# Optimization experiments

Measured on AMD Instinct MI355X. Metric: run time of the kernel, lower is better.

The kernel has to match this reference:

```python
import jax, jax.numpy as jnp
import numpy as np

B, S, L, H, D, FF, V = 2, 1024, 12, 12, 768, 3072, 50265
DH = D // H
W1 = 256                      # one-sided window (attention_window=512)
MOTIF = (31 + 96 + 80) * 2    # 414
MAXPOS = 4098
EPS = 1e-5
NEG = jnp.float32(-1e9)


def _ln(x, s, b):
    m = jnp.mean(x, -1, keepdims=True)
    v = jnp.mean(jnp.square(x - m), -1, keepdims=True)
    return (x - m) * jax.lax.rsqrt(v + EPS) * s + b


def setup_inputs() -> dict:
    key = jax.random.key(0)
    ks = iter(jax.random.split(key, 48))
    n = lambda *sh: jax.random.normal(next(ks), sh, jnp.float32) * 0.02
    return {
        "input_ids": jax.random.randint(next(ks), (B, S), 0, V),
        "attention_mask": jnp.ones((B, S), jnp.int32),
        "motif_dist": jax.random.uniform(next(ks), (B, MOTIF), dtype=jnp.float32),
        "emb_word": n(V, D), "emb_pos": n(MAXPOS, D), "emb_type": n(1, D),
        "emb_ln_s": jnp.ones((D,)), "emb_ln_b": jnp.zeros((D,)),
        "Wq": n(L, D, D), "bq": jnp.zeros((L, D)),
        "Wk": n(L, D, D), "bk": jnp.zeros((L, D)),
        "Wv": n(L, D, D), "bv": jnp.zeros((L, D)),
        "Wqg": n(L, D, D), "bqg": jnp.zeros((L, D)),
        "Wkg": n(L, D, D), "bkg": jnp.zeros((L, D)),
        "Wvg": n(L, D, D), "bvg": jnp.zeros((L, D)),
        "Wo": n(L, D, D), "bo": jnp.zeros((L, D)),
        "ln1_s": jnp.ones((L, D)), "ln1_b": jnp.zeros((L, D)),
        "Wi": n(L, D, FF), "bi": jnp.zeros((L, FF)),
        "Wo2": n(L, FF, D), "bo2": jnp.zeros((L, D)),
        "ln2_s": jnp.ones((L, D)), "ln2_b": jnp.zeros((L, D)),
        "head_Wd": n(D + MOTIF, D), "head_bd": jnp.zeros((D,)),
        "head_Wp": n(D, 2), "head_bp": jnp.zeros((2,)),
    }


def reference(input_ids, attention_mask, motif_dist, emb_word, emb_pos, emb_type,
              emb_ln_s, emb_ln_b, Wq, bq, Wk, bk, Wv, bv, Wqg, bqg, Wkg, bkg,
              Wvg, bvg, Wo, bo, ln1_s, ln1_b, Wi, bi, Wo2, bo2, ln2_s, ln2_b,
              head_Wd, head_bd, head_Wp, head_bp):
    Bn, Sn = input_ids.shape
    scale = 1.0 / np.sqrt(DH)
    # RoBERTa-style embeddings: positions start at padding_idx+1 = 2
    pos_ids = jnp.arange(Sn) + 2
    x = emb_word[input_ids] + emb_pos[pos_ids][None] + emb_type[0][None, None]
    x = _ln(x, emb_ln_s, emb_ln_b)

    key_valid = attention_mask.astype(bool)[:, None, None, :]      # [B,1,1,S]
    idx = jnp.arange(Sn)
    is_global = idx == 0                                           # default: CLS-only global
    band = jnp.abs(idx[:, None] - idx[None, :]) <= W1
    # local query attends to its sliding window plus all global keys
    local_allowed = (band | is_global[None, :])[None, None] & key_valid

    def heads(t, s):
        return t.reshape(Bn, s, H, DH).transpose(0, 2, 1, 3)       # [B,H,s,DH]

    for l in range(L):
        q = heads(x @ Wq[l] + bq[l], Sn) * scale
        k = heads(x @ Wk[l] + bk[l], Sn)
        v = heads(x @ Wv[l] + bv[l], Sn)
        scores = jnp.einsum('bhid,bhjd->bhij', q, k)
        probs = jax.nn.softmax(jnp.where(local_allowed, scores, NEG), -1)
        out = jnp.einsum('bhij,bhjd->bhid', probs, v)              # [B,H,S,DH]
        # global (CLS) query: full attention using the *_global projections
        qg = heads(x[:, :1] @ Wqg[l] + bqg[l], 1) * scale          # [B,H,1,DH]
        kg = heads(x @ Wkg[l] + bkg[l], Sn)
        vg = heads(x @ Wvg[l] + bvg[l], Sn)
        sg = jnp.einsum('bhid,bhjd->bhij', qg, kg)                 # [B,H,1,S]
        pg = jax.nn.softmax(jnp.where(key_valid, sg, NEG), -1)
        og = jnp.einsum('bhij,bhjd->bhid', pg, vg)                 # [B,H,1,DH]
        out = jnp.concatenate([og, out[:, :, 1:]], axis=2)
        out = out.transpose(0, 2, 1, 3).reshape(Bn, Sn, D)
        x = _ln(x + out @ Wo[l] + bo[l], ln1_s[l], ln1_b[l])
        h = jax.nn.gelu(x @ Wi[l] + bi[l], approximate=False)
        x = _ln(x + h @ Wo2[l] + bo2[l], ln2_s[l], ln2_b[l])

    # classification head: CLS hidden state concat motif distribution
    hcat = jnp.concatenate([x[:, 0, :], motif_dist], axis=-1)
    return jnp.tanh(hcat @ head_Wd + head_bd) @ head_Wp + head_bp
```

## Files before the change

kernel.cpp:

```cpp
#include <hip/hip_runtime.h>
#include <math.h>

typedef unsigned short u16;
typedef __attribute__((ext_vector_type(8))) short short8;
typedef __attribute__((ext_vector_type(4))) float f32x4;

#define BB 2
#define SS 1024
#define LL 12
#define HH 12
#define DD 768
#define FFF 3072
#define MOTIF 414
#define HCAT (DD + MOTIF)
#define W1 256
#define NEGV -1e9f
#define EPS 1e-5f
#define SCALE 0.125f
#define LD5 3840
#define WL_ELE 8257536

__device__ __forceinline__ float bf2f(u16 u) {
    union { unsigned i; float f; } x; x.i = ((unsigned)u) << 16; return x.f;
}
__device__ __forceinline__ u16 f2bf(float f) {
    union { float f; unsigned i; } x; x.f = f;
    unsigned r = x.i + 0x7fffu + ((x.i >> 16) & 1u);
    return (u16)(r >> 16);
}

__device__ __forceinline__ void gld16(const u16* g, u16* l) {
    __builtin_amdgcn_global_load_lds((const __attribute__((address_space(1))) void*)g,
                                     (__attribute__((address_space(3))) void*)l, 16, 0, 0);
}

__device__ __forceinline__ float block_reduce_sum(float v, float* red) {
    int t = threadIdx.x;
    red[t] = v; __syncthreads();
    #pragma unroll
    for (int s = 128; s > 0; s >>= 1) {
        if (t < s) red[t] += red[t + s];
        __syncthreads();
    }
    float r = red[0]; __syncthreads();
    return r;
}

__global__ __launch_bounds__(256) void embed_ln_kernel(
    const int* __restrict__ ids, const float* __restrict__ ew,
    const float* __restrict__ ep, const float* __restrict__ et,
    const float* __restrict__ gs, const float* __restrict__ gb,
    float* __restrict__ X, u16* __restrict__ Xb) {
    __shared__ float red[256];
    int row = blockIdx.x;
    int s = row % SS;
    int id = ids[row];
    int t = threadIdx.x;
    float v[3];
    float sum = 0.f;
    #pragma unroll
    for (int i = 0; i < 3; ++i) {
        int d = t + 256 * i;
        float x = ew[(size_t)id * DD + d] + ep[(size_t)(s + 2) * DD + d] + et[d];
        v[i] = x; sum += x;
    }
    sum = block_reduce_sum(sum, red);
    float m = sum * (1.f / DD);
    float sq = 0.f;
    #pragma unroll
    for (int i = 0; i < 3; ++i) { float c = v[i] - m; sq += c * c; }
    sq = block_reduce_sum(sq, red);
    float inv = rsqrtf(sq * (1.f / DD) + EPS);
    #pragma unroll
    for (int i = 0; i < 3; ++i) {
        int d = t + 256 * i;
        float o = (v[i] - m) * inv * gs[d] + gb[d];
        X[(size_t)row * DD + d] = o;
        Xb[(size_t)row * DD + d] = f2bf(o);
    }
}

__global__ __launch_bounds__(256) void add_ln_kernel(
    float* __restrict__ X, u16* __restrict__ Xb,
    const float* __restrict__ Tbase, int NT,
    const float* __restrict__ gs, const float* __restrict__ gb) {
    __shared__ float red[256];
    int row = blockIdx.x;
    int t = threadIdx.x;
    const size_t MN = (size_t)BB * SS * DD;
    float v[3];
    float sum = 0.f;
    #pragma unroll
    for (int i = 0; i < 3; ++i) {
        int d = t + 256 * i;
        size_t idx = (size_t)row * DD + d;
        float x = X[idx];
        for (int p = 0; p < NT; ++p) x += Tbase[p * MN + idx];
        v[i] = x; sum += x;
    }
    sum = block_reduce_sum(sum, red);
    float m = sum * (1.f / DD);
    float sq = 0.f;
    #pragma unroll
    for (int i = 0; i < 3; ++i) { float c = v[i] - m; sq += c * c; }
    sq = block_reduce_sum(sq, red);
    float inv = rsqrtf(sq * (1.f / DD) + EPS);
    #pragma unroll
    for (int i = 0; i < 3; ++i) {
        int d = t + 256 * i;
        float o = (v[i] - m) * inv * gs[d] + gb[d];
        X[(size_t)row * DD + d] = o;
        Xb[(size_t)row * DD + d] = f2bf(o);
    }
}

template <int LAYERED>
__global__ __launch_bounds__(256) void conv_all_kernel(
    const float* __restrict__ Wqp, const float* __restrict__ Wkp,
    const float* __restrict__ Wvp, const float* __restrict__ Wkgp,
    const float* __restrict__ Wvgp, const float* __restrict__ Wop,
    const float* __restrict__ Wip, const float* __restrict__ Wo2p,
    u16* __restrict__ WtBase) {
    __shared__ float Tt[64][33];
    int l = LAYERED ? blockIdx.y : 0;
    size_t oDD = (size_t)l * DD * DD;
    size_t oFF = (size_t)l * DD * FFF;
    u16* Wt6  = WtBase + (size_t)l * WL_ELE;
    u16* Wti  = Wt6 + 6 * DD * DD;
    u16* Wto2 = Wti + FFF * DD;
    int tid = blockIdx.x;
    const float* W; u16* Wt; int Nd, Kd, n0, k0;
    if (tid < 1728) {
        int z = tid / 288, rem = tid % 288;
        const float* w6[6] = {Wqp + oDD, Wkp + oDD, Wvp + oDD, Wkgp + oDD, Wvgp + oDD, Wop + oDD};
        W = w6[z];
        Wt = Wt6 + (size_t)z * DD * DD;
        Nd = DD; Kd = DD; n0 = (rem % 24) * 32; k0 = (rem / 24) * 64;
    } else if (tid < 2880) {
        int i = tid - 1728;
        W = Wip + oFF; Wt = Wti; Nd = FFF; Kd = DD; n0 = (i % 96) * 32; k0 = (i / 96) * 64;
    } else {
        int i = tid - 2880;
        W = Wo2p + oFF; Wt = Wto2; Nd = DD; Kd = FFF; n0 = (i % 24) * 32; k0 = (i / 24) * 64;
    }
    int t = threadIdx.x;
    int r = t >> 3, c = (t & 7) * 4;
    #pragma unroll
    for (int half = 0; half < 2; ++half) {
        float4 v = *(const float4*)(W + (size_t)(k0 + half * 32 + r) * Nd + n0 + c);
        Tt[half * 32 + r][c + 0] = v.x;
        Tt[half * 32 + r][c + 1] = v.y;
        Tt[half * 32 + r][c + 2] = v.z;
        Tt[half * 32 + r][c + 3] = v.w;
    }
    __syncthreads();
    int n = t >> 3, kk = (t & 7) * 8;
    union { uint4 v; u16 e[8]; } wv;
    #pragma unroll
    for (int j = 0; j < 8; ++j) wv.e[j] = f2bf(Tt[kk + j][n]);
    *(uint4*)&Wt[(size_t)(n0 + n) * Kd + k0 + kk] = wv.v;
}

__global__ __launch_bounds__(256) void bcat_kernel(
    const float* __restrict__ bq, const float* __restrict__ bk,
    const float* __restrict__ bv, const float* __restrict__ bkg,
    const float* __restrict__ bvg, float* __restrict__ bcat) {
    int tid = blockIdx.x * 256 + threadIdx.x;
    if (tid >= LL * LD5) return;
    int l = tid / LD5, r = tid % LD5, z = r / DD, j = r % DD;
    const float* src = (z == 0) ? bq : (z == 1) ? bk : (z == 2) ? bv : (z == 3) ? bkg : bvg;
    bcat[tid] = src[l * DD + j];
}

#define STAGE(j, buf)                                                                   \
    do {                                                                                \
        int _k0 = (j) << 5;                                                             \
        _Pragma("unroll")                                                               \
        for (int _op = 0; _op < 2; ++_op) {                                             \
            int _rc = rA + _op * 16;                                                    \
            int _r = _rc + rr;                                                          \
            gld16(A  + (size_t)(bm + _r) * K + kbeg + _k0 + ((s4 ^ (_r & 3)) * 8),      \
                  &As[buf][_rc * 32]);                                                  \
            gld16(Bt + (size_t)(bn + _r) * K + kbeg + _k0 + ((s4 ^ (_r & 3)) * 8),      \
                  &Bs[buf][_rc * 32]);                                                  \
        }                                                                               \
    } while (0)

template <int ACT, int OBF>
__global__ __launch_bounds__(256) void gemm_bf16(
    const u16* __restrict__ A, const u16* __restrict__ Bt,
    const float* __restrict__ bias, void* __restrict__ Cout,
    int M, int N, int K, int Ksplit) {
    __shared__ __align__(16) u16 As[3][128 * 32];
    __shared__ __align__(16) u16 Bs[3][128 * 32];
    int z = blockIdx.z;
    int kbeg = z * Ksplit;
    int kend = kbeg + Ksplit; if (kend > K) kend = K;
    int t = threadIdx.x, lane = t & 63, wv = t >> 6;
    int bm = blockIdx.y * 128, bn = blockIdx.x * 128;
    int wm = wv >> 1, wn = wv & 1;
    int h = lane >> 4, q15 = lane & 15;
    int rA = wv * 32;
    int rr = lane >> 2, s4 = lane & 3;
    f32x4 acc[4][4];
    #pragma unroll
    for (int i = 0; i < 4; ++i)
        #pragma unroll
        for (int j = 0; j < 4; ++j) { acc[i][j][0] = 0.f; acc[i][j][1] = 0.f; acc[i][j][2] = 0.f; acc[i][j][3] = 0.f; }

    int nk = (kend - kbeg) >> 5;
    STAGE(0, 0);
    if (nk > 1) STAGE(1, 1);
    if (nk > 2) STAGE(2, 2);
    int cur = 0;
    for (int i = 0; i < nk; ++i) {
        int ahead = nk - 1 - i;
        if (ahead >= 2)      asm volatile("s_waitcnt vmcnt(8)" ::: "memory");
        else if (ahead == 1) asm volatile("s_waitcnt vmcnt(4)" ::: "memory");
        else                 asm volatile("s_waitcnt vmcnt(0)" ::: "memory");
        __builtin_amdgcn_s_barrier();
        short8 af[4], bfr[4];
        #pragma unroll
        for (int mf = 0; mf < 4; ++mf) {
            int row = wm * 64 + mf * 16 + q15;
            af[mf] = *(const short8*)&As[cur][row * 32 + ((h ^ (row & 3)) * 8)];
        }
        #pragma unroll
        for (int nf = 0; nf < 4; ++nf) {
            int row = wn * 64 + nf * 16 + q15;
            bfr[nf] = *(const short8*)&Bs[cur][row * 32 + ((h ^ (row & 3)) * 8)];
        }
        asm volatile("s_waitcnt lgkmcnt(0)" ::: "memory");
        __builtin_amdgcn_sched_barrier(0);
        __builtin_amdgcn_s_barrier();
        __builtin_amdgcn_sched_barrier(0);
        if (i + 3 < nk) STAGE(i + 3, cur);
        #pragma unroll
        for (int mf = 0; mf < 4; ++mf)
            #pragma unroll
            for (int nf = 0; nf < 4; ++nf)
                acc[mf][nf] = __builtin_amdgcn_mfma_f32_16x16x32_bf16(af[mf], bfr[nf], acc[mf][nf], 0, 0, 0);
        cur = (cur == 2) ? 0 : cur + 1;
    }
    float* Cf = (float*)Cout + (size_t)z * M * N;
    u16*   Cb = (u16*)Cout;
    #pragma unroll
    for (int mf = 0; mf < 4; ++mf) {
        int mbase = bm + wm * 64 + mf * 16 + h * 4;
        #pragma unroll
        for (int nf = 0; nf < 4; ++nf) {
            int n = bn + wn * 64 + nf * 16 + q15;
            float bv = 0.f;
            if (z == 0) bv = bias[n];
            #pragma unroll
            for (int rg = 0; rg < 4; ++rg) {
                float val = acc[mf][nf][rg] + bv;
                if (ACT == 1) val = 0.5f * val * (1.f + erff(val * 0.70710678118654752f));
                if (OBF) Cb[(size_t)(mbase + rg) * N + n] = f2bf(val);
                else     Cf[(size_t)(mbase + rg) * N + n] = val;
            }
        }
    }
}

__global__ __launch_bounds__(256) void attn_local_mfma(
    const u16* __restrict__ QKV, const int* __restrict__ mask,
    u16* __restrict__ AO) {
    __shared__ __align__(16) u16 Qs[64 * 64];
    __shared__ __align__(16) u16 Ks[2][64 * 64];
    __shared__ __align__(16) u16 Vst[2][64 * 64];
    __shared__ __align__(16) u16 Pld[4][16 * 64];
    __shared__ float mskAll[SS];
    int bid = blockIdx.x;
    int qt = bid & 15;
    int hh = (bid >> 4) % HH;
    int b  = bid / (16 * HH);
    int t = threadIdx.x, lane = t & 63, wv = t >> 6;
    int h = lane >> 4, q15 = lane & 15;
    int i0 = qt * 64;

    int jlo = i0 - W1; if (jlo < 0) jlo = 0;
    int jend = i0 + 64 + W1; if (jend > SS) jend = SS;
    int hasCLS = (jlo > 0) ? 1 : 0;
    int nt = hasCLS + (jend - jlo) / 64;
    int iq = i0 + wv * 16 + q15;

    {
        int4 mi = *(const int4*)&mask[b * SS + t * 4];
        mskAll[t * 4 + 0] = (float)mi.x;
        mskAll[t * 4 + 1] = (float)mi.y;
        mskAll[t * 4 + 2] = (float)mi.z;
        mskAll[t * 4 + 3] = (float)mi.w;
    }
    #pragma unroll
    for (int op = 0; op < 2; ++op) {
        int r = wv * 16 + op * 8 + (lane >> 3), s = lane & 7;
        gld16(QKV + (size_t)(b * SS + i0 + r) * LD5 + hh * 64 + ((s ^ (r & 7)) * 8),
              &Qs[(wv * 16 + op * 8) * 64]);
    }
    int base0 = hasCLS ? 0 : jlo;
    #pragma unroll
    for (int op = 0; op < 2; ++op) {
        int r = wv * 16 + op * 8 + (lane >> 3), s = lane & 7;
        gld16(QKV + (size_t)(b * SS + base0 + r) * LD5 + 768 + hh * 64 + ((s ^ (r & 7)) * 8),
              &Ks[0][(wv * 16 + op * 8) * 64]);
    }
    int k2 = t & 31, dsec = t >> 5;
    union { uint4 v; u16 e[8]; } vr0, vr1;
    {
        const u16* vp = QKV + (size_t)(b * SS + base0 + 2 * k2) * LD5 + 1536 + hh * 64 + dsec * 8;
        vr0.v = *(const uint4*)vp;
        vr1.v = *(const uint4*)(vp + LD5);
    }
    asm volatile("s_waitcnt vmcnt(0)" ::: "memory");
    {
        int slot = k2 >> 2;
        #pragma unroll
        for (int j = 0; j < 8; ++j) {
            int d = dsec * 8 + j;
            unsigned val = (unsigned)vr0.e[j] | ((unsigned)vr1.e[j] << 16);
            *(unsigned*)&Vst[0][d * 64 + ((slot ^ (d & 7)) * 8) + ((2 * k2) & 7)] = val;
        }
    }
    __syncthreads();
    short8 bq[2];
    {
        int qrow = wv * 16 + q15;
        #pragma unroll
        for (int ks = 0; ks < 2; ++ks)
            bq[ks] = *(const short8*)&Qs[qrow * 64 + (((ks * 4 + h) ^ (qrow & 7)) * 8)];
    }

    float mrun = -3e38f, lrun = 0.f;
    f32x4 o[4];
    #pragma unroll
    for (int nf = 0; nf < 4; ++nf) { o[nf][0] = 0.f; o[nf][1] = 0.f; o[nf][2] = 0.f; o[nf][3] = 0.f; }

    for (int tt = 0; tt < nt; ++tt) {
        int cur = tt & 1, nxt = cur ^ 1;
        int base = (hasCLS && tt == 0) ? 0 : jlo + (tt - hasCLS) * 64;
        if (tt + 1 < nt) {
            int basen = jlo + (tt + 1 - hasCLS) * 64;
            #pragma unroll
            for (int op = 0; op < 2; ++op) {
                int r = wv * 16 + op * 8 + (lane >> 3), s = lane & 7;
                gld16(QKV + (size_t)(b * SS + basen + r) * LD5 + 768 + hh * 64 + ((s ^ (r & 7)) * 8),
                      &Ks[nxt][(wv * 16 + op * 8) * 64]);
            }
            const u16* vp = QKV + (size_t)(b * SS + basen + 2 * k2) * LD5 + 1536 + hh * 64 + dsec * 8;
            vr0.v = *(const uint4*)vp;
            vr1.v = *(const uint4*)(vp + LD5);
        }

        f32x4 sacc[4];
        #pragma unroll
        for (int kf = 0; kf < 4; ++kf) { sacc[kf][0] = 0.f; sacc[kf][1] = 0.f; sacc[kf][2] = 0.f; sacc[kf][3] = 0.f; }
        #pragma unroll
        for (int ks = 0; ks < 2; ++ks) {
            #pragma unroll
            for (int kf = 0; kf < 4; ++kf) {
                int krow = kf * 16 + q15;
                short8 afr = *(const short8*)&Ks[cur][krow * 64 + (((ks * 4 + h) ^ (krow & 7)) * 8)];
                sacc[kf] = __builtin_amdgcn_mfma_f32_16x16x32_bf16(afr, bq[ks], sacc[kf], 0, 0, 0);
            }
        }
        float pv[4][4];
        float tmax = -3e38f;
        #pragma unroll
        for (int kf = 0; kf < 4; ++kf) {
            #pragma unroll
            for (int rg = 0; rg < 4; ++rg) {
                int kl = kf * 16 + h * 4 + rg;
                int key = base + kl;
                int dj = iq - key; int adj = dj < 0 ? -dj : dj;
                bool valid = ((adj <= W1) || (key == 0)) && (mskAll[key] != 0.f);
                float s = valid ? sacc[kf][rg] * SCALE : NEGV;
                pv[kf][rg] = s;
                tmax = fmaxf(tmax, s);
            }
        }
        tmax = fmaxf(tmax, __shfl_xor(tmax, 16));
        tmax = fmaxf(tmax, __shfl_xor(tmax, 32));
        float mnew = fmaxf(mrun, tmax);
        float fac = __expf(mrun - mnew);
        mrun = mnew;
        float psum = 0.f;
        #pragma unroll
        for (int kf = 0; kf < 4; ++kf)
            #pragma unroll
            for (int rg = 0; rg < 4; ++rg) {
                float p = __expf(pv[kf][rg] - mnew);
                pv[kf][rg] = p; psum += p;
            }
        psum += __shfl_xor(psum, 16);
        psum += __shfl_xor(psum, 32);
        lrun = lrun * fac + psum;
        #pragma unroll
        for (int kf = 0; kf < 4; ++kf) {
            unsigned lo = (unsigned)f2bf(pv[kf][0]) | ((unsigned)f2bf(pv[kf][1]) << 16);
            unsigned hi = (unsigned)f2bf(pv[kf][2]) | ((unsigned)f2bf(pv[kf][3]) << 16);
            int slot = 2 * kf + (h >> 1);
            uint2 w; w.x = lo; w.y = hi;
            *(uint2*)&Pld[wv][q15 * 64 + ((slot ^ (q15 & 7)) * 8) + 4 * (h & 1)] = w;
        }
        float fo0 = __shfl(fac, (h * 4 + 0) | (lane & 48));
        float fo1 = __shfl(fac, (h * 4 + 1) | (lane & 48));
        float fo2 = __shfl(fac, (h * 4 + 2) | (lane & 48));
        float fo3 = __shfl(fac, (h * 4 + 3) | (lane & 48));
        #pragma unroll
        for (int nf = 0; nf < 4; ++nf) {
            o[nf][0] *= fo0; o[nf][1] *= fo1; o[nf][2] *= fo2; o[nf][3] *= fo3;
        }
        asm volatile("s_waitcnt lgkmcnt(0)" ::: "memory");
        #pragma unroll
        for (int ks = 0; ks < 2; ++ks) {
            short8 ap = *(const short8*)&Pld[wv][q15 * 64 + (((ks * 4 + h) ^ (q15 & 7)) * 8)];
            #pragma unroll
            for (int nf = 0; nf < 4; ++nf) {
                int d = nf * 16 + q15;
                short8 bvf = *(const short8*)&Vst[cur][d * 64 + (((ks * 4 + h) ^ (d & 7)) * 8)];
                o[nf] = __builtin_amdgcn_mfma_f32_16x16x32_bf16(ap, bvf, o[nf], 0, 0, 0);
            }
        }
        if (tt + 1 < nt) {
            asm volatile("s_waitcnt vmcnt(0)" ::: "memory");
            int slot = k2 >> 2;
            #pragma unroll
            for (int j = 0; j < 8; ++j) {
                int d = dsec * 8 + j;
                unsigned val = (unsigned)vr0.e[j] | ((unsigned)vr1.e[j] << 16);
                *(unsigned*)&Vst[nxt][d * 64 + ((slot ^ (d & 7)) * 8) + ((2 * k2) & 7)] = val;
            }
            __syncthreads();
        }
    }
    float linv = 1.f / lrun;
    float g0 = __shfl(linv, (h * 4 + 0) | (lane & 48));
    float g1 = __shfl(linv, (h * 4 + 1) | (lane & 48));
    float g2 = __shfl(linv, (h * 4 + 2) | (lane & 48));
    float g3 = __shfl(linv, (h * 4 + 3) | (lane & 48));
    size_t rb = (size_t)(b * SS + i0 + wv * 16 + h * 4);
    #pragma unroll
    for (int nf = 0; nf < 4; ++nf) {
        int d = hh * 64 + nf * 16 + q15;
        AO[(rb + 0) * DD + d] = f2bf(o[nf][0] * g0);
        AO[(rb + 1) * DD + d] = f2bf(o[nf][1] * g1);
        AO[(rb + 2) * DD + d] = f2bf(o[nf][2] * g2);
        AO[(rb + 3) * DD + d] = f2bf(o[nf][3] * g3);
    }
}

__global__ __launch_bounds__(512) void attn_global_kernel(
    const float* __restrict__ Xf, const float* __restrict__ Wqg,
    const float* __restrict__ bqg, const u16* __restrict__ QKV,
    const int* __restrict__ mask, u16* __restrict__ AO) {
    __shared__ float x0[DD];
    __shared__ float qv[64];
    __shared__ float sc[SS];
    __shared__ float red[512];
    __shared__ float part[8][64];
    int b = blockIdx.x / HH, hh = blockIdx.x % HH;
    int t = threadIdx.x;
    for (int i = t; i < DD; i += 512) x0[i] = Xf[(size_t)b * SS * DD + i];
    __syncthreads();
    {
        int d = t & 63, p = t >> 6;
        float acc = 0.f;
        int k0 = p * 96;
        #pragma unroll 8
        for (int k = k0; k < k0 + 96; ++k)
            acc += x0[k] * Wqg[(size_t)k * DD + hh * 64 + d];
        part[p][d] = acc;
    }
    __syncthreads();
    if (t < 64) {
        float s = bqg[hh * 64 + t];
        #pragma unroll
        for (int p = 0; p < 8; ++p) s += part[p][t];
        qv[t] = s * SCALE;
    }
    __syncthreads();
    for (int j = t; j < SS; j += 512) {
        const u16* kp = QKV + (size_t)(b * SS + j) * LD5 + 2304 + hh * 64;
        float acc = 0.f;
        #pragma unroll
        for (int d0 = 0; d0 < 64; d0 += 8) {
            union { uint4 v; u16 e[8]; } u;
            u.v = *(const uint4*)(kp + d0);
            #pragma unroll
            for (int j2 = 0; j2 < 8; ++j2) acc += qv[d0 + j2] * bf2f(u.e[j2]);
        }
        sc[j] = mask[b * SS + j] ? acc : NEGV;
    }
    __syncthreads();
    float mx = fmaxf(sc[t], sc[t + 512]);
    red[t] = mx; __syncthreads();
    #pragma unroll
    for (int s = 256; s > 0; s >>= 1) {
        if (t < s) red[t] = fmaxf(red[t], red[t + s]);
        __syncthreads();
    }
    mx = red[0]; __syncthreads();
    float e0 = __expf(sc[t] - mx), e1 = __expf(sc[t + 512] - mx);
    sc[t] = e0; sc[t + 512] = e1;
    red[t] = e0 + e1; __syncthreads();
    #pragma unroll
    for (int s = 256; s > 0; s >>= 1) {
        if (t < s) red[t] += red[t + s];
        __syncthreads();
    }
    float lsum = red[0]; __syncthreads();
    int g = t >> 6, d = t & 63;
    float acc = 0.f;
    for (int j = g; j < SS; j += 8)
        acc += sc[j] * bf2f(QKV[(size_t)(b * SS + j) * LD5 + 3072 + hh * 64 + d]);
    part[g][d] = acc;
    __syncthreads();
    if (g == 0) {
        float ov = 0.f;
        #pragma unroll
        for (int p = 0; p < 8; ++p) ov += part[p][d];
        AO[(size_t)(b * SS) * DD + hh * 64 + d] = f2bf(ov / lsum);
    }
}

__global__ __launch_bounds__(256) void head1_kernel(
    const float* __restrict__ X, const float* __restrict__ motif,
    const float* __restrict__ Wd, float* __restrict__ hpart) {
    __shared__ float hc[HCAT];
    __shared__ float part[4][64];
    int jb = blockIdx.x, kp = blockIdx.y, b = blockIdx.z;
    int t = threadIdx.x;
    for (int i = t; i < DD; i += 256) hc[i] = X[(size_t)b * SS * DD + i];
    for (int i = t; i < MOTIF; i += 256) hc[DD + i] = motif[(size_t)b * MOTIF + i];
    __syncthreads();
    int j = jb * 64 + (t & 63);
    int sub = t >> 6;
    int k0 = kp * 148 + sub * 37;
    int k1 = k0 + 37; if (k1 > HCAT) k1 = HCAT;
    float acc = 0.f;
    for (int k = k0; k < k1; ++k) acc += hc[k] * Wd[(size_t)k * DD + j];
    part[sub][t & 63] = acc;
    __syncthreads();
    if (sub == 0) {
        int x = t & 63;
        hpart[((size_t)b * 8 + kp) * DD + j] = part[0][x] + part[1][x] + part[2][x] + part[3][x];
    }
}

__global__ __launch_bounds__(256) void head2_kernel(
    const float* __restrict__ hpart, const float* __restrict__ bd,
    const float* __restrict__ Wp, const float* __restrict__ bp,
    float* __restrict__ out) {
    __shared__ float dvs[DD];
    __shared__ float red[256];
    int b = blockIdx.x;
    int t = threadIdx.x;
    for (int j = t; j < DD; j += 256) {
        float s = bd[j];
        #pragma unroll
        for (int kp = 0; kp < 8; ++kp) s += hpart[((size_t)b * 8 + kp) * DD + j];
        dvs[j] = tanhf(s);
    }
    __syncthreads();
    float a0 = 0.f, a1 = 0.f;
    for (int k = t; k < DD; k += 256) {
        a0 += dvs[k] * Wp[k * 2 + 0];
        a1 += dvs[k] * Wp[k * 2 + 1];
    }
    a0 = block_reduce_sum(a0, red);
    a1 = block_reduce_sum(a1, red);
    if (t == 0) {
        out[b * 2 + 0] = a0 + bp[0];
        out[b * 2 + 1] = a1 + bp[1];
    }
}

extern "C" void kernel_launch(void* const* d_in, const int* in_sizes, int n_in,
                              void* d_out, int out_size, void* d_ws, size_t ws_size,
                              hipStream_t stream) {
    const int*   input_ids = (const int*)d_in[0];
    const int*   attn_mask = (const int*)d_in[1];
    const float* motif     = (const float*)d_in[2];
    const float* emb_word  = (const float*)d_in[3];
    const float* emb_pos   = (const float*)d_in[4];
    const float* emb_type  = (const float*)d_in[5];
    const float* emb_ln_s  = (const float*)d_in[6];
    const float* emb_ln_b  = (const float*)d_in[7];
    const float* Wq  = (const float*)d_in[8];
    const float* bq  = (const float*)d_in[9];
    const float* Wk  = (const float*)d_in[10];
    const float* bk  = (const float*)d_in[11];
    const float* Wv  = (const float*)d_in[12];
    const float* bv  = (const float*)d_in[13];
    const float* Wqg = (const float*)d_in[14];
    const float* bqg = (const float*)d_in[15];
    const float* Wkg = (const float*)d_in[16];
    const float* bkg = (const float*)d_in[17];
    const float* Wvg = (const float*)d_in[18];
    const float* bvg = (const float*)d_in[19];
    const float* Wo  = (const float*)d_in[20];
    const float* bo  = (const float*)d_in[21];
    const float* ln1_s = (const float*)d_in[22];
    const float* ln1_b = (const float*)d_in[23];
    const float* Wi  = (const float*)d_in[24];
    const float* bi  = (const float*)d_in[25];
    const float* Wo2 = (const float*)d_in[26];
    const float* bo2 = (const float*)d_in[27];
    const float* ln2_s = (const float*)d_in[28];
    const float* ln2_b = (const float*)d_in[29];
    const float* head_Wd = (const float*)d_in[30];
    const float* head_bd = (const float*)d_in[31];
    const float* head_Wp = (const float*)d_in[32];
    const float* head_bp = (const float*)d_in[33];

    float* out = (float*)d_out;
    char* base = (char*)d_ws;

    float* Xf   = (float*)(base + 0);
    u16*   Xb   = (u16*)  (base + 6291456);
    u16*   QKVb = (u16*)  (base + 9437184);
    u16*   AOb  = (u16*)  (base + 25165824);
    float* T1f  = (float*)(base + 28311552);

    const size_t NEED_BIG  = 70225920;
    const size_t NEED_HUGE = 251891712;
    bool huge = ws_size >= NEED_HUGE;
    bool big  = huge || ws_size >= NEED_BIG;
    int NT = big ? 4 : 1;

    u16* WtAll; float* bcat; float* hpart;
    u16 *Wt6_s = nullptr, *Wti_s = nullptr, *Wto2_s = nullptr;
    if (huge) {
        bcat  = (float*)(base + 53477376);
        hpart = (float*)(base + 53661696);
        WtAll = (u16*)  (base + 53710848);
    } else {
        size_t wbase = big ? 53710848 : 34603008;
        Wt6_s  = (u16*)(base + wbase);
        Wti_s  = (u16*)(base + wbase + 7077888);
        Wto2_s = (u16*)(base + wbase + 11796480);
        bcat   = (float*)(base + wbase + 16515072);
        hpart  = (float*)(base + wbase + 16699392);
        WtAll  = Wt6_s;
    }
    u16* Hb = QKVb;

    const int nrow = BB * SS;

    embed_ln_kernel<<<nrow, 256, 0, stream>>>(input_ids, emb_word, emb_pos, emb_type,
                                              emb_ln_s, emb_ln_b, Xf, Xb);
    bcat_kernel<<<(LL * LD5 + 255) / 256, 256, 0, stream>>>(bq, bk, bv, bkg, bvg, bcat);
    if (huge)
        conv_all_kernel<1><<<dim3(4032, 12), 256, 0, stream>>>(
            Wq, Wk, Wv, Wkg, Wvg, Wo, Wi, Wo2, WtAll);

    dim3 g5(30, 16, 1);
    dim3 gO(6, 16, NT);
    dim3 gFF1(24, 16, 1);
    dim3 gFF2(6, 16, NT);

    for (int l = 0; l < LL; ++l) {
        size_t oDD = (size_t)l * DD * DD;
        u16 *Wt6, *Wti, *Wto2;
        if (huge) {
            Wt6  = WtAll + (size_t)l * WL_ELE;
            Wti  = Wt6 + 6 * DD * DD;
            Wto2 = Wti + FFF * DD;
        } else {
            conv_all_kernel<0><<<dim3(4032, 1), 256, 0, stream>>>(
                Wq + oDD, Wk + oDD, Wv + oDD, Wkg + oDD, Wvg + oDD, Wo + oDD,
                Wi + (size_t)l * DD * FFF, Wo2 + (size_t)l * FFF * DD, Wt6_s);
            Wt6 = Wt6_s; Wti = Wti_s; Wto2 = Wto2_s;
        }

        gemm_bf16<0, 1><<<g5, 256, 0, stream>>>(Xb, Wt6, bcat + l * LD5, QKVb,
                                                nrow, LD5, DD, DD);

        attn_local_mfma<<<BB * HH * 16, 256, 0, stream>>>(QKVb, attn_mask, AOb);
        attn_global_kernel<<<BB * HH, 512, 0, stream>>>(Xf, Wqg + oDD, bqg + l * DD,
                                                        QKVb, attn_mask, AOb);

        gemm_bf16<0, 0><<<gO, 256, 0, stream>>>(AOb, Wt6 + 5 * (size_t)DD * DD, bo + l * DD,
                                                T1f, nrow, DD, DD, DD / NT);
        add_ln_kernel<<<nrow, 256, 0, stream>>>(Xf, Xb, T1f, NT,
                                                ln1_s + l * DD, ln1_b + l * DD);

        gemm_bf16<1, 1><<<gFF1, 256, 0, stream>>>(Xb, Wti, bi + l * FFF, Hb,
                                                  nrow, FFF, DD, DD);
        gemm_bf16<0, 0><<<gFF2, 256, 0, stream>>>(Hb, Wto2, bo2 + l * DD,
                                                  T1f, nrow, DD, FFF, FFF / NT);
        add_ln_kernel<<<nrow, 256, 0, stream>>>(Xf, Xb, T1f, NT,
                                                ln2_s + l * DD, ln2_b + l * DD);
    }

    head1_kernel<<<dim3(12, 8, BB), 256, 0, stream>>>(Xf, motif, head_Wd, hpart);
    head2_kernel<<<BB, 256, 0, stream>>>(hpart, head_bd, head_Wp, head_bp, out);
}
```

Baseline: 2.444 ms.

## Remap GEMM workgroups per XCD and switch to double-buffered LDS pipeline

Flattens the GEMM grid to one dimension and remaps block IDs so consecutive tiles land on the same XCD, grouping M tiles that share a weight column tile to improve L2 reuse. It also shrinks the LDS pipeline from three stages to two, with a peeled final iteration. The smaller LDS footprint may allow more resident blocks per CU, but prefetch depth drops and global-load latency may be hidden less well.

```diff
diff --git a/kernel.cpp b/kernel.cpp
--- a/kernel.cpp
+++ b/kernel.cpp
@@ -190,14 +190,20 @@
 __global__ __launch_bounds__(256) void gemm_bf16(
     const u16* __restrict__ A, const u16* __restrict__ Bt,
     const float* __restrict__ bias, void* __restrict__ Cout,
-    int M, int N, int K, int Ksplit) {
-    __shared__ __align__(16) u16 As[3][128 * 32];
-    __shared__ __align__(16) u16 Bs[3][128 * 32];
-    int z = blockIdx.z;
+    int M, int N, int K, int Ksplit, int GY) {
+    __shared__ __align__(16) u16 As[2][128 * 32];
+    __shared__ __align__(16) u16 Bs[2][128 * 32];
+    int nwg = gridDim.x;
+    int orig = blockIdx.x;
+    int q = nwg >> 3, r8 = nwg & 7;
+    int xcd = orig & 7;
+    int wgid = (xcd < r8 ? xcd * (q + 1) : r8 * (q + 1) + (xcd - r8) * q) + (orig >> 3);
+    int bn = (wgid / GY) * 128;
+    int bm = (wgid % GY) * 128;
+    int z = blockIdx.y;
     int kbeg = z * Ksplit;
     int kend = kbeg + Ksplit; if (kend > K) kend = K;
     int t = threadIdx.x, lane = t & 63, wv = t >> 6;
-    int bm = blockIdx.y * 128, bn = blockIdx.x * 128;
     int wm = wv >> 1, wn = wv & 1;
     int h = lane >> 4, q15 = lane & 15;
     int rA = wv * 32;
@@ -211,13 +217,9 @@
     int nk = (kend - kbeg) >> 5;
     STAGE(0, 0);
     if (nk > 1) STAGE(1, 1);
-    if (nk > 2) STAGE(2, 2);
     int cur = 0;
-    for (int i = 0; i < nk; ++i) {
-        int ahead = nk - 1 - i;
-        if (ahead >= 2)      asm volatile("s_waitcnt vmcnt(8)" ::: "memory");
-        else if (ahead == 1) asm volatile("s_waitcnt vmcnt(4)" ::: "memory");
-        else                 asm volatile("s_waitcnt vmcnt(0)" ::: "memory");
+    for (int i = 0; i < nk - 1; ++i) {
+        asm volatile("s_waitcnt vmcnt(4)" ::: "memory");
         __builtin_amdgcn_s_barrier();
         short8 af[4], bfr[4];
         #pragma unroll
@@ -234,13 +236,33 @@
         __builtin_amdgcn_sched_barrier(0);
         __builtin_amdgcn_s_barrier();
         __builtin_amdgcn_sched_barrier(0);
-        if (i + 3 < nk) STAGE(i + 3, cur);
+        if (i + 2 < nk) STAGE(i + 2, cur);
         #pragma unroll
         for (int mf = 0; mf < 4; ++mf)
             #pragma unroll
             for (int nf = 0; nf < 4; ++nf)
                 acc[mf][nf] = __builtin_amdgcn_mfma_f32_16x16x32_bf16(af[mf], bfr[nf], acc[mf][nf], 0, 0, 0);
-        cur = (cur == 2) ? 0 : cur + 1;
+        cur ^= 1;
+    }
+    asm volatile("s_waitcnt vmcnt(0)" ::: "memory");
+    __builtin_amdgcn_s_barrier();
+    {
+        short8 af[4], bfr[4];
+        #pragma unroll
+        for (int mf = 0; mf < 4; ++mf) {
+            int row = wm * 64 + mf * 16 + q15;
+            af[mf] = *(const short8*)&As[cur][row * 32 + ((h ^ (row & 3)) * 8)];
+        }
+        #pragma unroll
+        for (int nf = 0; nf < 4; ++nf) {
+            int row = wn * 64 + nf * 16 + q15;
+            bfr[nf] = *(const short8*)&Bs[cur][row * 32 + ((h ^ (row & 3)) * 8)];
+        }
+        #pragma unroll
+        for (int mf = 0; mf < 4; ++mf)
+            #pragma unroll
+            for (int nf = 0; nf < 4; ++nf)
+                acc[mf][nf] = __builtin_amdgcn_mfma_f32_16x16x32_bf16(af[mf], bfr[nf], acc[mf][nf], 0, 0, 0);
     }
     float* Cf = (float*)Cout + (size_t)z * M * N;
     u16*   Cb = (u16*)Cout;
@@ -655,10 +677,10 @@
         conv_all_kernel<1><<<dim3(4032, 12), 256, 0, stream>>>(
             Wq, Wk, Wv, Wkg, Wvg, Wo, Wi, Wo2, WtAll);
 
-    dim3 g5(30, 16, 1);
-    dim3 gO(6, 16, NT);
-    dim3 gFF1(24, 16, 1);
-    dim3 gFF2(6, 16, NT);
+    dim3 g5(480, 1);
+    dim3 gO(96, NT);
+    dim3 gFF1(384, 1);
+    dim3 gFF2(96, NT);
 
     for (int l = 0; l < LL; ++l) {
         size_t oDD = (size_t)l * DD * DD;
@@ -675,21 +697,21 @@
         }
 
         gemm_bf16<0, 1><<<g5, 256, 0, stream>>>(Xb, Wt6, bcat + l * LD5, QKVb,
-                                                nrow, LD5, DD, DD);
+                                                nrow, LD5, DD, DD, 16);
 
         attn_local_mfma<<<BB * HH * 16, 256, 0, stream>>>(QKVb, attn_mask, AOb);
         attn_global_kernel<<<BB * HH, 512, 0, stream>>>(Xf, Wqg + oDD, bqg + l * DD,
                                                         QKVb, attn_mask, AOb);
 
         gemm_bf16<0, 0><<<gO, 256, 0, stream>>>(AOb, Wt6 + 5 * (size_t)DD * DD, bo + l * DD,
-                                                T1f, nrow, DD, DD, DD / NT);
+                                                T1f, nrow, DD, DD, DD / NT, 16);
         add_ln_kernel<<<nrow, 256, 0, stream>>>(Xf, Xb, T1f, NT,
                                                 ln1_s + l * DD, ln1_b + l * DD);
 
         gemm_bf16<1, 1><<<gFF1, 256, 0, stream>>>(Xb, Wti, bi + l * FFF, Hb,
-                                                  nrow, FFF, DD, DD);
+                                                  nrow, FFF, DD, DD, 16);
         gemm_bf16<0, 0><<<gFF2, 256, 0, stream>>>(Hb, Wto2, bo2 + l * DD,
-                                                  T1f, nrow, DD, FFF, FFF / NT);
+                                                  T1f, nrow, DD, FFF, FFF / NT, 16);
         add_ln_kernel<<<nrow, 256, 0, stream>>>(Xf, Xb, T1f, NT,
                                                 ln2_s + l * DD, ln2_b + l * DD);
     }
```

Result: no change. 2.478 ms (+1.4%).
